# Optimization experiments

Hardware: AMD Instinct MI355X
Metric: run time of the kernel (lower is better)

## Reference

```python
import jax, jax.numpy as jnp
import numpy as np

TOKEN_NUM = 81   # init default token_num
KNN_K = 2        # hardcoded in apply_clustering
LAYER_INDEX = 3


def setup_inputs() -> dict:
    key = jax.random.key(0)
    k1, k2, k3 = jax.random.split(key, 3)
    B, F, N, C = 8, 1024, 17, 512
    x = jax.random.normal(k1, (B, F, N, C), dtype=jnp.float32)
    # nn.Parameter init normal_(std=0.02)
    pos_embed_token = 0.02 * jax.random.normal(k2, (1, TOKEN_NUM, C), dtype=jnp.float32)
    # deterministic stand-in for torch.rand tie-breaker noise on density
    density_noise = jax.random.uniform(k3, (B, F), dtype=jnp.float32)
    return {"x": x, "pos_embed_token": pos_embed_token,
            "density_noise": density_noise, "current_layer": LAYER_INDEX}


def _dpc_knn_index(x_knn, density_noise, cluster_num, k):
    # x_knn: (B, F, C) pooled features; returns sorted cluster-center indices (B, cluster_num)
    B, F, C = x_knn.shape
    sq = jnp.sum(x_knn * x_knn, axis=-1)                       # (B, F)
    d2 = sq[:, :, None] + sq[:, None, :] - 2.0 * jnp.einsum('bic,bjc->bij', x_knn, x_knn)
    dist = jnp.sqrt(jnp.maximum(d2, 0.0)) / jnp.sqrt(jnp.asarray(C, x_knn.dtype))  # cdist / C**0.5
    # k smallest distances (self included, dist 0)
    neg_nearest, _ = jax.lax.top_k(-dist, k)                   # (B, F, k)
    dist_nearest = -neg_nearest
    density = jnp.exp(-jnp.mean(dist_nearest ** 2, axis=-1))   # (B, F)
    density = density + density_noise * 1e-6                   # tie-breaker
    # mask[b,i,j] = density[b,j] > density[b,i]
    mask = (density[:, None, :] > density[:, :, None]).astype(x_knn.dtype)
    dist_max = jnp.max(dist.reshape(B, -1), axis=-1)[:, None, None]
    min_dist = jnp.min(dist * mask + dist_max * (1.0 - mask), axis=-1)  # (B, F)
    score = min_dist * density
    _, index_down = jax.lax.top_k(score, cluster_num)          # (B, cluster_num)
    return jnp.sort(index_down, axis=-1)


def reference(x, pos_embed_token, density_noise, current_layer):
    # forward path only hits clustering when current_layer == layer_index
    if current_layer != LAYER_INDEX:
        return x
    B, F, N, C = x.shape
    # AdaptiveAvgPool1d(1) over joint axis after 'b f n c -> b (f c) n' == mean over n
    x_knn = jnp.mean(x, axis=2)                                # (B, F, C)
    index = _dpc_knn_index(x_knn, density_noise, TOKEN_NUM, KNN_K)
    index = jax.lax.stop_gradient(index)                       # clustering is under no_grad
    # gather selected frames: x[batch, index] -> (B, token_num, N, C)
    compressed = jnp.take_along_axis(x, index[:, :, None, None], axis=1)
    # '+ pos_embed_token' applied per (b n) f c  ==  broadcast over joints
    compressed = compressed + pos_embed_token[:, :, None, :]
    return compressed
```

## Files before the change

### kernel.cpp

```cpp
#include <hip/hip_runtime.h>
#include <math.h>
#include <float.h>

#define BB 8
#define FF 1024
#define NJ 17
#define CH 512
#define TOK 81
#define RCP_SQRT_C 0.04419417382415922f
#define LP 133

typedef short bf16x8 __attribute__((ext_vector_type(8)));
typedef float f32x16 __attribute__((ext_vector_type(16)));

static __device__ inline unsigned short f2bf(float f) {
    __bf16 h = (__bf16)f;
    return __builtin_bit_cast(unsigned short, h);
}
static __device__ inline float bf2f(unsigned short u) {
    return (float)__builtin_bit_cast(__bf16, u);
}


__global__ __launch_bounds__(256) void pool_kernel(const float* __restrict__ x,
                                                   uint4* __restrict__ fhi,
                                                   uint4* __restrict__ flo,
                                                   float* __restrict__ sq,
                                                   unsigned* __restrict__ dmx) {
    const int t = threadIdx.x;
    if (blockIdx.x == 0 && t < BB) dmx[t] = 0u;
    const int wid = t >> 6, lane = t & 63;
    const int row0 = blockIdx.x * 4;
    const int row = row0 + wid;
    const int b = row >> 10, f0 = row0 & 1023;
    const float* px = x + (size_t)row * NJ * CH + lane * 8;
    float a[8] = {};
    #pragma unroll
    for (int n = 0; n < NJ; ++n) {
        const float4 v0 = *(const float4*)(px + (size_t)n * CH);
        const float4 v1 = *(const float4*)(px + (size_t)n * CH + 4);
        a[0] += v0.x; a[1] += v0.y; a[2] += v0.z; a[3] += v0.w;
        a[4] += v1.x; a[5] += v1.y; a[6] += v1.z; a[7] += v1.w;
    }
    float ssq = 0.f;
    unsigned short hi[8], lo[8];
    #pragma unroll
    for (int j = 0; j < 8; ++j) {
        const float m = a[j] / 17.0f;
        ssq += m * m;
        hi[j] = f2bf(m);
        lo[j] = f2bf(m - bf2f(hi[j]));
    }
    #pragma unroll
    for (int off = 32; off > 0; off >>= 1) ssq += __shfl_down(ssq, off);
    if (lane == 0) sq[row] = ssq;

    uint4 uh, ul;
    uh.x = (unsigned)hi[0] | ((unsigned)hi[1] << 16);
    uh.y = (unsigned)hi[2] | ((unsigned)hi[3] << 16);
    uh.z = (unsigned)hi[4] | ((unsigned)hi[5] << 16);
    uh.w = (unsigned)hi[6] | ((unsigned)hi[7] << 16);
    ul.x = (unsigned)lo[0] | ((unsigned)lo[1] << 16);
    ul.y = (unsigned)lo[2] | ((unsigned)lo[3] << 16);
    ul.z = (unsigned)lo[4] | ((unsigned)lo[5] << 16);
    ul.w = (unsigned)lo[6] | ((unsigned)lo[7] << 16);
    __shared__ uint4 sh_hi[256], sh_lo[256];
    sh_hi[lane * 4 + wid] = uh;
    sh_lo[lane * 4 + wid] = ul;
    __syncthreads();
    const int k8 = t >> 2, fpr = t & 3;
    const int s = k8 >> 1, h = k8 & 1;
    const size_t o = (((size_t)b * 32 + s) * 2 + h) * 1024 + f0 + fpr;
    fhi[o] = sh_hi[t];
    flo[o] = sh_lo[t];
}

__global__ __launch_bounds__(256) void dist_kernel(const uint4* __restrict__ fhi,
                                                   const uint4* __restrict__ flo,
                                                   const float* __restrict__ sq,
                                                   float* __restrict__ dist) {
    const int b = blockIdx.x & 7;
    int tri = blockIdx.x >> 3, rt = 0;
    while (tri >= 8 - rt) { tri -= 8 - rt; ++rt; }
    const int ct = rt + tri;
    const bool diag = (rt == ct);
    const int tid = threadIdx.x;
    const int w = tid >> 6, lane = tid & 63;
    const int R = rt * 128 + (w & 1) * 64;
    const int C = ct * 128 + (w >> 1) * 64;
    const int h = lane >> 5, fr = lane & 31;

    size_t a0 = ((size_t)b * 64 + h) * 1024 + R + fr;
    size_t b0 = ((size_t)b * 64 + h) * 1024 + C + fr;

    f32x16 acc00, acc01, acc10, acc11;
    #pragma unroll
    for (int i = 0; i < 16; ++i) { acc00[i] = 0.f; acc01[i] = 0.f; acc10[i] = 0.f; acc11[i] = 0.f; }

    bf16x8 A0h = *(const bf16x8*)(fhi + a0), A1h = *(const bf16x8*)(fhi + a0 + 32);
    bf16x8 A0l = *(const bf16x8*)(flo + a0), A1l = *(const bf16x8*)(flo + a0 + 32);
    bf16x8 B0h = *(const bf16x8*)(fhi + b0), B1h = *(const bf16x8*)(fhi + b0 + 32);
    bf16x8 B0l = *(const bf16x8*)(flo + b0), B1l = *(const bf16x8*)(flo + b0 + 32);

    #pragma unroll 4
    for (int s = 0; s < 32; ++s) {
        const bf16x8 cA0h = A0h, cA1h = A1h, cA0l = A0l, cA1l = A1l;
        const bf16x8 cB0h = B0h, cB1h = B1h, cB0l = B0l, cB1l = B1l;
        if (s < 31) {
            a0 += 2048; b0 += 2048;
            A0h = *(const bf16x8*)(fhi + a0); A1h = *(const bf16x8*)(fhi + a0 + 32);
            A0l = *(const bf16x8*)(flo + a0); A1l = *(const bf16x8*)(flo + a0 + 32);
            B0h = *(const bf16x8*)(fhi + b0); B1h = *(const bf16x8*)(fhi + b0 + 32);
            B0l = *(const bf16x8*)(flo + b0); B1l = *(const bf16x8*)(flo + b0 + 32);
        }
        acc00 = __builtin_amdgcn_mfma_f32_32x32x16_bf16(cA0h, cB0h, acc00, 0, 0, 0);
        acc01 = __builtin_amdgcn_mfma_f32_32x32x16_bf16(cA0h, cB1h, acc01, 0, 0, 0);
        acc10 = __builtin_amdgcn_mfma_f32_32x32x16_bf16(cA1h, cB0h, acc10, 0, 0, 0);
        acc11 = __builtin_amdgcn_mfma_f32_32x32x16_bf16(cA1h, cB1h, acc11, 0, 0, 0);
        acc00 = __builtin_amdgcn_mfma_f32_32x32x16_bf16(cA0h, cB0l, acc00, 0, 0, 0);
        acc01 = __builtin_amdgcn_mfma_f32_32x32x16_bf16(cA0h, cB1l, acc01, 0, 0, 0);
        acc10 = __builtin_amdgcn_mfma_f32_32x32x16_bf16(cA1h, cB0l, acc10, 0, 0, 0);
        acc11 = __builtin_amdgcn_mfma_f32_32x32x16_bf16(cA1h, cB1l, acc11, 0, 0, 0);
        acc00 = __builtin_amdgcn_mfma_f32_32x32x16_bf16(cA0l, cB0h, acc00, 0, 0, 0);
        acc01 = __builtin_amdgcn_mfma_f32_32x32x16_bf16(cA0l, cB1h, acc01, 0, 0, 0);
        acc10 = __builtin_amdgcn_mfma_f32_32x32x16_bf16(cA1l, cB0h, acc10, 0, 0, 0);
        acc11 = __builtin_amdgcn_mfma_f32_32x32x16_bf16(cA1l, cB1h, acc11, 0, 0, 0);
    }

    __shared__ float lds[64 * LP];
    const int bF = b * FF;
    const int R0 = rt * 128, C0 = ct * 128;
    const float sqc0 = sq[bF + C + fr], sqc1 = sq[bF + C + fr + 32];
    const int lcb = (w >> 1) * 64 + fr;

    #pragma unroll
    for (int p = 0; p < 2; ++p) {
        if ((w & 1) == p) {
            #pragma unroll
            for (int reg = 0; reg < 16; ++reg) {
                const int rp = 4 * h + (reg & 3) + 8 * (reg >> 2);
                const float sqr0 = sq[bF + R + rp];
                const float sqr1 = sq[bF + R + rp + 32];
                lds[rp * LP + lcb] =
                    sqrtf(fmaxf(sqr0 + sqc0 - 2.0f * acc00[reg], 0.f)) * RCP_SQRT_C;
                lds[rp * LP + lcb + 32] =
                    sqrtf(fmaxf(sqr0 + sqc1 - 2.0f * acc01[reg], 0.f)) * RCP_SQRT_C;
                lds[(rp + 32) * LP + lcb] =
                    sqrtf(fmaxf(sqr1 + sqc0 - 2.0f * acc10[reg], 0.f)) * RCP_SQRT_C;
                lds[(rp + 32) * LP + lcb + 32] =
                    sqrtf(fmaxf(sqr1 + sqc1 - 2.0f * acc11[reg], 0.f)) * RCP_SQRT_C;
            }
        }
        __syncthreads();
        if (!diag) {
            for (int q = tid; q < 64 * 128; q += 256) {
                const int lr = q >> 7, c = q & 127;
                dist[((size_t)bF + R0 + p * 64 + lr) * FF + C0 + c] = lds[lr * LP + c];
            }
            for (int q = tid; q < 64 * 128; q += 256) {
                const int lr = q & 63, c = q >> 6;
                dist[((size_t)bF + C0 + c) * FF + R0 + p * 64 + lr] = lds[lr * LP + c];
            }
        } else if (p == 0) {
            for (int q = tid; q < 64 * 128; q += 256) {
                const int i = q >> 7, j = q & 127;
                const float v = (i == j) ? 0.f : (i < j ? lds[i * LP + j] : lds[j * LP + i]);
                dist[((size_t)bF + R0 + i) * FF + C0 + j] = v;
            }
            for (int q = tid; q < 64 * 64; q += 256) {
                const int i = 64 + (q >> 6), j = q & 63;
                dist[((size_t)bF + R0 + i) * FF + C0 + j] = lds[j * LP + i];
            }
        } else {
            for (int q = tid; q < 64 * 64; q += 256) {
                const int i = 64 + (q >> 6), j = 64 + (q & 63);
                const float v = (i == j) ? 0.f
                               : (i < j ? lds[(i - 64) * LP + j] : lds[(j - 64) * LP + i]);
                dist[((size_t)bF + R0 + i) * FF + C0 + j] = v;
            }
        }
        __syncthreads();
    }
}

__device__ inline void merge2(float& lo0, float& lo1, float c0, float c1) {
    float n0 = fminf(lo0, c0);
    float n1 = fminf(fmaxf(lo0, c0), fminf(lo1, c1));
    lo0 = n0; lo1 = n1;
}

__global__ __launch_bounds__(256) void rowstat_kernel(const float* __restrict__ dist,
                                                      const float* __restrict__ noise,
                                                      float* __restrict__ density,
                                                      unsigned* __restrict__ dmx) {
    const int wid = threadIdx.x >> 6;
    const int r = blockIdx.x * 4 + wid;
    const int lane = threadIdx.x & 63;
    const float* dr = dist + (size_t)r * FF + lane * 4;
    float lo0 = FLT_MAX, lo1 = FLT_MAX, mx = -FLT_MAX;
    #pragma unroll
    for (int j = 0; j < 4; ++j) {
        const float4 d = *(const float4*)(dr + j * 256);
        mx = fmaxf(mx, fmaxf(fmaxf(d.x, d.y), fmaxf(d.z, d.w)));
        merge2(lo0, lo1, fminf(d.x, d.y), fmaxf(d.x, d.y));
        merge2(lo0, lo1, fminf(d.z, d.w), fmaxf(d.z, d.w));
    }
    #pragma unroll
    for (int off = 32; off > 0; off >>= 1) {
        const float o0 = __shfl_down(lo0, off);
        const float o1 = __shfl_down(lo1, off);
        const float om = __shfl_down(mx, off);
        merge2(lo0, lo1, o0, o1);
        mx = fmaxf(mx, om);
    }
    __shared__ float wmx[4];
    if (lane == 0) {
        density[r] = expf(-0.5f * (lo0 * lo0 + lo1 * lo1)) + noise[r] * 1e-6f;
        wmx[wid] = mx;
    }
    __syncthreads();
    if (threadIdx.x == 0) {
        const float m = fmaxf(fmaxf(wmx[0], wmx[1]), fmaxf(wmx[2], wmx[3]));
        atomicMax(&dmx[blockIdx.x >> 8], __float_as_uint(m));
    }
}

__global__ __launch_bounds__(256) void scoremin_kernel(const float* __restrict__ dist,
                                                       const float* __restrict__ density,
                                                       const float* __restrict__ distmax,
                                                       float* __restrict__ score) {
    const int r = blockIdx.x * 4 + (threadIdx.x >> 6);
    const int lane = threadIdx.x & 63;
    const int b = r >> 10;
    const float* dr = dist + (size_t)r * FF + lane * 4;
    const float* db = density + (size_t)b * FF + lane * 4;
    const float dme = density[r];
    float mn = FLT_MAX;
    #pragma unroll
    for (int j = 0; j < 4; ++j) {
        const float4 d = *(const float4*)(dr + j * 256);
        const float4 de = *(const float4*)(db + j * 256);
        mn = fminf(mn, (de.x > dme) ? d.x : FLT_MAX);
        mn = fminf(mn, (de.y > dme) ? d.y : FLT_MAX);
        mn = fminf(mn, (de.z > dme) ? d.z : FLT_MAX);
        mn = fminf(mn, (de.w > dme) ? d.w : FLT_MAX);
    }
    #pragma unroll
    for (int off = 32; off > 0; off >>= 1) mn = fminf(mn, __shfl_down(mn, off));
    if (lane == 0) {
        if (mn == FLT_MAX) mn = distmax[b];
        score[r] = mn * dme;
    }
}

__global__ __launch_bounds__(256) void topk_kernel(const float* __restrict__ score,
                                                   int* __restrict__ selsort) {
    const int b = blockIdx.x, t = threadIdx.x;
    const int w = t >> 6, lane = t & 63;
    const float* sb = score + b * FF;
    unsigned v[4];
    #pragma unroll
    for (int j = 0; j < 4; ++j) v[j] = __float_as_uint(sb[t + 256 * j]);

    __shared__ unsigned hist[256];
    __shared__ unsigned wtot[4];
    __shared__ unsigned sh_byte, sh_kk;
    unsigned prefix = 0, kk = TOK;
    #pragma unroll
    for (int pass = 0; pass < 4; ++pass) {
        const int sh = 24 - 8 * pass;
        const unsigned pmask = (pass == 0) ? 0u : (0xFFFFFFFFu << (sh + 8));
        hist[t] = 0;
        __syncthreads();
        #pragma unroll
        for (int j = 0; j < 4; ++j)
            if ((v[j] & pmask) == prefix) atomicAdd(&hist[(v[j] >> sh) & 255], 1u);
        __syncthreads();
        const unsigned cnt = hist[t];
        unsigned s = cnt;
        #pragma unroll
        for (int off = 1; off < 64; off <<= 1) {
            const unsigned o = __shfl_down(s, off);
            if (lane + off < 64) s += o;
        }
        if (lane == 0) wtot[w] = s;
        __syncthreads();
        unsigned hi2 = 0;
        for (int w2 = w + 1; w2 < 4; ++w2) hi2 += wtot[w2];
        const unsigned S_incl = s + hi2;
        const unsigned S_excl = S_incl - cnt;
        if (S_excl < kk && kk <= S_incl) { sh_byte = (unsigned)t; sh_kk = kk - S_excl; }
        __syncthreads();
        prefix |= (sh_byte << sh);
        kk = sh_kk;
    }
    const unsigned T = prefix;

    __shared__ unsigned cgt[16], ceq[16];
    unsigned long long bgt[4], beq[4];
    #pragma unroll
    for (int j = 0; j < 4; ++j) {
        bgt[j] = __ballot(v[j] > T);
        beq[j] = __ballot(v[j] == T);
        if (lane == 0) {
            cgt[j * 4 + w] = (unsigned)__popcll(bgt[j]);
            ceq[j * 4 + w] = (unsigned)__popcll(beq[j]);
        }
    }
    __syncthreads();
    const unsigned long long below = (1ULL << lane) - 1ULL;
    #pragma unroll
    for (int j = 0; j < 4; ++j) {
        const bool gt = v[j] > T, eq = v[j] == T;
        if (!gt && !eq) continue;
        const int c = j * 4 + w;
        unsigned bq_gt = 0, bq_eq = 0;
        for (int cc = 0; cc < c; ++cc) { bq_gt += cgt[cc]; bq_eq += ceq[cc]; }
        const unsigned wgt = (unsigned)__popcll(bgt[j] & below);
        const unsigned weq = (unsigned)__popcll(beq[j] & below);
        unsigned pos;
        if (gt) {
            const unsigned eq_before = bq_eq + weq;
            pos = bq_gt + wgt + ((eq_before < kk) ? eq_before : kk);
        } else {
            const unsigned e = bq_eq + weq;
            if (e >= kk) continue;
            pos = bq_gt + wgt + e;
        }
        selsort[b * TOK + pos] = (int)(t + 256 * j);
    }
}

__global__ __launch_bounds__(256) void gather_kernel(const float* __restrict__ x,
                                                     const float* __restrict__ pos,
                                                     const int* __restrict__ selsort,
                                                     float* __restrict__ out) {
    const size_t i = (size_t)blockIdx.x * 256 + threadIdx.x;
    const size_t total = (size_t)BB * TOK * NJ * (CH / 4);
    if (i >= total) return;
    const int c4 = (int)(i & (CH / 4 - 1));
    size_t r = i >> 7;
    const int n = (int)(r % NJ); r /= NJ;
    const int t = (int)(r % TOK);
    const int b = (int)(r / TOK);
    const int f = selsort[b * TOK + t];
    float4 v = *(const float4*)(x + (((size_t)(b * FF + f)) * NJ + n) * CH + c4 * 4);
    const float4 p = *(const float4*)(pos + (size_t)t * CH + c4 * 4);
    v.x += p.x; v.y += p.y; v.z += p.z; v.w += p.w;
    *(float4*)(out + i * 4) = v;
}

extern "C" void kernel_launch(void* const* d_in, const int* in_sizes, int n_in,
                              void* d_out, int out_size, void* d_ws, size_t ws_size,
                              hipStream_t stream) {
    const float* x     = (const float*)d_in[0];
    const float* pos   = (const float*)d_in[1];
    const float* noise = (const float*)d_in[2];
    float* out = (float*)d_out;

    uint4* fhi    = (uint4*)d_ws;
    uint4* flo    = fhi + (size_t)BB * 32 * 2 * 1024;
    float* dist   = (float*)(flo + (size_t)BB * 32 * 2 * 1024);
    float* sq     = dist + (size_t)BB * FF * FF;
    float* density = sq + BB * FF;
    float* distmax = density + BB * FF;
    float* score   = distmax + 8;
    int*   selsort = (int*)(score + BB * FF);

    pool_kernel<<<(BB * FF) / 4, 256, 0, stream>>>(x, fhi, flo, sq, (unsigned*)distmax);
    dist_kernel<<<288, 256, 0, stream>>>(fhi, flo, sq, dist);
    rowstat_kernel<<<(BB * FF) / 4, 256, 0, stream>>>(dist, noise, density, (unsigned*)distmax);
    scoremin_kernel<<<(BB * FF) / 4, 256, 0, stream>>>(dist, density, distmax, score);
    topk_kernel<<<BB, 256, 0, stream>>>(score, selsort);
    const int gtot = (int)(((size_t)BB * TOK * NJ * (CH / 4) + 255) / 256);
    gather_kernel<<<gtot, 256, 0, stream>>>(x, pos, selsort, out);
}
```

Measured before the change: 483.4 us.

## Fuse row stats, score, top-k and gather into one persistent kernel

```diff
diff --git a/kernel.cpp b/kernel.cpp
--- a/kernel.cpp
+++ b/kernel.cpp
@@ -26,9 +26,9 @@
                                                    uint4* __restrict__ fhi,
                                                    uint4* __restrict__ flo,
                                                    float* __restrict__ sq,
-                                                   unsigned* __restrict__ dmx) {
+                                                   unsigned* __restrict__ ctrl) {
     const int t = threadIdx.x;
-    if (blockIdx.x == 0 && t < BB) dmx[t] = 0u;
+    if (blockIdx.x == 0 && t < 24) ctrl[t] = 0u;
     const int wid = t >> 6, lane = t & 63;
     const int row0 = blockIdx.x * 4;
     const int row = row0 + wid;
@@ -183,171 +183,200 @@
     }
 }
 
-__device__ inline void merge2(float& lo0, float& lo1, float c0, float c1) {
-    float n0 = fminf(lo0, c0);
-    float n1 = fminf(fmaxf(lo0, c0), fminf(lo1, c1));
-    lo0 = n0; lo1 = n1;
-}
-
-__global__ __launch_bounds__(256) void rowstat_kernel(const float* __restrict__ dist,
-                                                      const float* __restrict__ noise,
-                                                      float* __restrict__ density,
-                                                      unsigned* __restrict__ dmx) {
-    const int wid = threadIdx.x >> 6;
-    const int r = blockIdx.x * 4 + wid;
-    const int lane = threadIdx.x & 63;
-    const float* dr = dist + (size_t)r * FF + lane * 4;
-    float lo0 = FLT_MAX, lo1 = FLT_MAX, mx = -FLT_MAX;
-    #pragma unroll
-    for (int j = 0; j < 4; ++j) {
-        const float4 d = *(const float4*)(dr + j * 256);
-        mx = fmaxf(mx, fmaxf(fmaxf(d.x, d.y), fmaxf(d.z, d.w)));
-        merge2(lo0, lo1, fminf(d.x, d.y), fmaxf(d.x, d.y));
-        merge2(lo0, lo1, fminf(d.z, d.w), fmaxf(d.z, d.w));
-    }
-    #pragma unroll
-    for (int off = 32; off > 0; off >>= 1) {
-        const float o0 = __shfl_down(lo0, off);
-        const float o1 = __shfl_down(lo1, off);
-        const float om = __shfl_down(mx, off);
-        merge2(lo0, lo1, o0, o1);
-        mx = fmaxf(mx, om);
-    }
-    __shared__ float wmx[4];
-    if (lane == 0) {
-        density[r] = expf(-0.5f * (lo0 * lo0 + lo1 * lo1)) + noise[r] * 1e-6f;
-        wmx[wid] = mx;
-    }
-    __syncthreads();
-    if (threadIdx.x == 0) {
-        const float m = fmaxf(fmaxf(wmx[0], wmx[1]), fmaxf(wmx[2], wmx[3]));
-        atomicMax(&dmx[blockIdx.x >> 8], __float_as_uint(m));
-    }
-}
-
-__global__ __launch_bounds__(256) void scoremin_kernel(const float* __restrict__ dist,
-                                                       const float* __restrict__ density,
-                                                       const float* __restrict__ distmax,
-                                                       float* __restrict__ score) {
-    const int r = blockIdx.x * 4 + (threadIdx.x >> 6);
-    const int lane = threadIdx.x & 63;
-    const int b = r >> 10;
-    const float* dr = dist + (size_t)r * FF + lane * 4;
-    const float* db = density + (size_t)b * FF + lane * 4;
-    const float dme = density[r];
-    float mn = FLT_MAX;
-    #pragma unroll
-    for (int j = 0; j < 4; ++j) {
-        const float4 d = *(const float4*)(dr + j * 256);
-        const float4 de = *(const float4*)(db + j * 256);
-        mn = fminf(mn, (de.x > dme) ? d.x : FLT_MAX);
-        mn = fminf(mn, (de.y > dme) ? d.y : FLT_MAX);
-        mn = fminf(mn, (de.z > dme) ? d.z : FLT_MAX);
-        mn = fminf(mn, (de.w > dme) ? d.w : FLT_MAX);
-    }
-    #pragma unroll
-    for (int off = 32; off > 0; off >>= 1) mn = fminf(mn, __shfl_down(mn, off));
-    if (lane == 0) {
-        if (mn == FLT_MAX) mn = distmax[b];
-        score[r] = mn * dme;
-    }
-}
-
-__global__ __launch_bounds__(256) void topk_kernel(const float* __restrict__ score,
-                                                   int* __restrict__ selsort) {
-    const int b = blockIdx.x, t = threadIdx.x;
-    const int w = t >> 6, lane = t & 63;
-    const float* sb = score + b * FF;
-    unsigned v[4];
-    #pragma unroll
-    for (int j = 0; j < 4; ++j) v[j] = __float_as_uint(sb[t + 256 * j]);
-
-    __shared__ unsigned hist[256];
-    __shared__ unsigned wtot[4];
-    __shared__ unsigned sh_byte, sh_kk;
-    unsigned prefix = 0, kk = TOK;
-    #pragma unroll
-    for (int pass = 0; pass < 4; ++pass) {
-        const int sh = 24 - 8 * pass;
-        const unsigned pmask = (pass == 0) ? 0u : (0xFFFFFFFFu << (sh + 8));
-        hist[t] = 0;
+__global__ __launch_bounds__(256) void stats_kernel(const float* __restrict__ dist,
+                                                    const float* __restrict__ noise,
+                                                    float* __restrict__ density,
+                                                    unsigned* __restrict__ ctrl,
+                                                    float* __restrict__ score,
+                                                    int* __restrict__ selsort,
+                                                    const float* __restrict__ x,
+                                                    const float* __restrict__ pos,
+                                                    float* __restrict__ out) {
+    const int t = threadIdx.x, wid = t >> 6, lane = t & 63;
+    const int g = blockIdx.x;
+    const int b = g >> 5;
+    unsigned* dmx = ctrl;
+    unsigned* syncA = ctrl + 8;
+    unsigned* syncD = ctrl + 9;
+    unsigned* bcnt  = ctrl + 10;
+
+    __shared__ float sdens[4][8];
+    float wmax = -FLT_MAX;
+    #pragma unroll
+    for (int k = 0; k < 8; ++k) {
+        const int r = g * 32 + wid * 8 + k;
+        const int dcol = r & 1023;
+        const float* dr = dist + (size_t)r * FF + lane * 4;
+        float mn = FLT_MAX, mx = -FLT_MAX;
+        #pragma unroll
+        for (int j = 0; j < 4; ++j) {
+            float4 d = *(const float4*)(dr + j * 256);
+            mx = fmaxf(mx, fmaxf(fmaxf(d.x, d.y), fmaxf(d.z, d.w)));
+            const int c0 = lane * 4 + j * 256;
+            d.x = (c0 + 0 == dcol) ? FLT_MAX : d.x;
+            d.y = (c0 + 1 == dcol) ? FLT_MAX : d.y;
+            d.z = (c0 + 2 == dcol) ? FLT_MAX : d.z;
+            d.w = (c0 + 3 == dcol) ? FLT_MAX : d.w;
+            mn = fminf(mn, fminf(fminf(d.x, d.y), fminf(d.z, d.w)));
+        }
+        #pragma unroll
+        for (int off = 32; off > 0; off >>= 1) {
+            mn = fminf(mn, __shfl_down(mn, off));
+            mx = fmaxf(mx, __shfl_down(mx, off));
+        }
+        if (lane == 0) {
+            const float dv = expf(-0.5f * mn * mn) + noise[r] * 1e-6f;
+            density[r] = dv;
+            sdens[wid][k] = dv;
+            wmax = fmaxf(wmax, mx);
+        }
+    }
+    __shared__ float swm[4];
+    if (lane == 0) swm[wid] = wmax;
+    __syncthreads();
+    if (t == 0) {
+        atomicMax(&dmx[b], __float_as_uint(fmaxf(fmaxf(swm[0], swm[1]), fmaxf(swm[2], swm[3]))));
+        __threadfence();
+        atomicAdd(syncA, 1u);
+        while (__hip_atomic_load(syncA, __ATOMIC_ACQUIRE, __HIP_MEMORY_SCOPE_AGENT) < 256u)
+            __builtin_amdgcn_s_sleep(8);
+    }
+    __syncthreads();
+    __threadfence();
+
+    const float dmaxb = __uint_as_float(
+        __hip_atomic_load(&dmx[b], __ATOMIC_RELAXED, __HIP_MEMORY_SCOPE_AGENT));
+    float e[16];
+    {
+        const volatile float* db = density + (size_t)b * FF;
+        #pragma unroll
+        for (int j = 0; j < 16; ++j) e[j] = db[lane + j * 64];
+    }
+    #pragma unroll
+    for (int k = 0; k < 8; ++k) {
+        const int r = g * 32 + wid * 8 + k;
+        const float dme = sdens[wid][k];
+        const float* dr = dist + (size_t)r * FF;
+        float mn = FLT_MAX;
+        #pragma unroll
+        for (int j = 0; j < 16; ++j) {
+            const float d = dr[lane + j * 64];
+            mn = fminf(mn, (e[j] > dme) ? d : FLT_MAX);
+        }
+        #pragma unroll
+        for (int off = 32; off > 0; off >>= 1) mn = fminf(mn, __shfl_down(mn, off));
+        if (lane == 0) score[r] = ((mn == FLT_MAX) ? dmaxb : mn) * dme;
+    }
+    __syncthreads();
+
+    __shared__ int slast;
+    if (t == 0) {
+        __threadfence();
+        slast = (atomicAdd(&bcnt[b], 1u) == 31u) ? 1 : 0;
+    }
+    __syncthreads();
+    if (slast) {
+        __threadfence();
+        const volatile float* sb = score + (size_t)b * FF;
+        unsigned v[4];
+        #pragma unroll
+        for (int j = 0; j < 4; ++j) v[j] = __float_as_uint(sb[t + 256 * j]);
+
+        __shared__ unsigned hist[256];
+        __shared__ unsigned wtot[4];
+        __shared__ unsigned sh_byte, sh_kk;
+        unsigned prefix = 0, kk = TOK;
+        #pragma unroll
+        for (int pass = 0; pass < 4; ++pass) {
+            const int sh = 24 - 8 * pass;
+            const unsigned pmask = (pass == 0) ? 0u : (0xFFFFFFFFu << (sh + 8));
+            hist[t] = 0;
+            __syncthreads();
+            #pragma unroll
+            for (int j = 0; j < 4; ++j)
+                if ((v[j] & pmask) == prefix) atomicAdd(&hist[(v[j] >> sh) & 255], 1u);
+            __syncthreads();
+            const unsigned cnt = hist[t];
+            unsigned s = cnt;
+            #pragma unroll
+            for (int off = 1; off < 64; off <<= 1) {
+                const unsigned o = __shfl_down(s, off);
+                if (lane + off < 64) s += o;
+            }
+            if (lane == 0) wtot[wid] = s;
+            __syncthreads();
+            unsigned hi2 = 0;
+            for (int w2 = wid + 1; w2 < 4; ++w2) hi2 += wtot[w2];
+            const unsigned S_incl = s + hi2;
+            const unsigned S_excl = S_incl - cnt;
+            if (S_excl < kk && kk <= S_incl) { sh_byte = (unsigned)t; sh_kk = kk - S_excl; }
+            __syncthreads();
+            prefix |= (sh_byte << sh);
+            kk = sh_kk;
+        }
+        const unsigned T = prefix;
+
+        __shared__ unsigned cgt[16], ceq[16];
+        unsigned long long bgt[4], beq[4];
+        #pragma unroll
+        for (int j = 0; j < 4; ++j) {
+            bgt[j] = __ballot(v[j] > T);
+            beq[j] = __ballot(v[j] == T);
+            if (lane == 0) {
+                cgt[j * 4 + wid] = (unsigned)__popcll(bgt[j]);
+                ceq[j * 4 + wid] = (unsigned)__popcll(beq[j]);
+            }
+        }
         __syncthreads();
-        #pragma unroll
-        for (int j = 0; j < 4; ++j)
-            if ((v[j] & pmask) == prefix) atomicAdd(&hist[(v[j] >> sh) & 255], 1u);
-        __syncthreads();
-        const unsigned cnt = hist[t];
-        unsigned s = cnt;
-        #pragma unroll
-        for (int off = 1; off < 64; off <<= 1) {
-            const unsigned o = __shfl_down(s, off);
-            if (lane + off < 64) s += o;
-        }
-        if (lane == 0) wtot[w] = s;
-        __syncthreads();
-        unsigned hi2 = 0;
-        for (int w2 = w + 1; w2 < 4; ++w2) hi2 += wtot[w2];
-        const unsigned S_incl = s + hi2;
-        const unsigned S_excl = S_incl - cnt;
-        if (S_excl < kk && kk <= S_incl) { sh_byte = (unsigned)t; sh_kk = kk - S_excl; }
-        __syncthreads();
-        prefix |= (sh_byte << sh);
-        kk = sh_kk;
-    }
-    const unsigned T = prefix;
-
-    __shared__ unsigned cgt[16], ceq[16];
-    unsigned long long bgt[4], beq[4];
-    #pragma unroll
-    for (int j = 0; j < 4; ++j) {
-        bgt[j] = __ballot(v[j] > T);
-        beq[j] = __ballot(v[j] == T);
-        if (lane == 0) {
-            cgt[j * 4 + w] = (unsigned)__popcll(bgt[j]);
-            ceq[j * 4 + w] = (unsigned)__popcll(beq[j]);
-        }
-    }
-    __syncthreads();
-    const unsigned long long below = (1ULL << lane) - 1ULL;
-    #pragma unroll
-    for (int j = 0; j < 4; ++j) {
-        const bool gt = v[j] > T, eq = v[j] == T;
-        if (!gt && !eq) continue;
-        const int c = j * 4 + w;
-        unsigned bq_gt = 0, bq_eq = 0;
-        for (int cc = 0; cc < c; ++cc) { bq_gt += cgt[cc]; bq_eq += ceq[cc]; }
-        const unsigned wgt = (unsigned)__popcll(bgt[j] & below);
-        const unsigned weq = (unsigned)__popcll(beq[j] & below);
-        unsigned pos;
-        if (gt) {
-            const unsigned eq_before = bq_eq + weq;
-            pos = bq_gt + wgt + ((eq_before < kk) ? eq_before : kk);
-        } else {
-            const unsigned e = bq_eq + weq;
-            if (e >= kk) continue;
-            pos = bq_gt + wgt + e;
-        }
-        selsort[b * TOK + pos] = (int)(t + 256 * j);
-    }
-}
-
-__global__ __launch_bounds__(256) void gather_kernel(const float* __restrict__ x,
-                                                     const float* __restrict__ pos,
-                                                     const int* __restrict__ selsort,
-                                                     float* __restrict__ out) {
-    const size_t i = (size_t)blockIdx.x * 256 + threadIdx.x;
+        const unsigned long long below = (1ULL << lane) - 1ULL;
+        #pragma unroll
+        for (int j = 0; j < 4; ++j) {
+            const bool gt = v[j] > T, eq = v[j] == T;
+            if (!gt && !eq) continue;
+            const int c = j * 4 + wid;
+            unsigned bq_gt = 0, bq_eq = 0;
+            for (int cc = 0; cc < c; ++cc) { bq_gt += cgt[cc]; bq_eq += ceq[cc]; }
+            const unsigned wgt = (unsigned)__popcll(bgt[j] & below);
+            const unsigned weq = (unsigned)__popcll(beq[j] & below);
+            unsigned pos_;
+            if (gt) {
+                const unsigned eq_before = bq_eq + weq;
+                pos_ = bq_gt + wgt + ((eq_before < kk) ? eq_before : kk);
+            } else {
+                const unsigned eord = bq_eq + weq;
+                if (eord >= kk) continue;
+                pos_ = bq_gt + wgt + eord;
+            }
+            selsort[b * TOK + pos_] = (int)(t + 256 * j);
+        }
+        __threadfence();
+    }
+    __syncthreads();
+    if (t == 0) atomicAdd(syncD, 1u);
+
+    if (t == 0) {
+        while (__hip_atomic_load(syncD, __ATOMIC_ACQUIRE, __HIP_MEMORY_SCOPE_AGENT) < 256u)
+            __builtin_amdgcn_s_sleep(8);
+    }
+    __syncthreads();
+    __threadfence();
+
+    __shared__ int ssel[BB * TOK];
+    for (int q = t; q < BB * TOK; q += 256) ssel[q] = *((volatile const int*)selsort + q);
+    __syncthreads();
     const size_t total = (size_t)BB * TOK * NJ * (CH / 4);
-    if (i >= total) return;
-    const int c4 = (int)(i & (CH / 4 - 1));
-    size_t r = i >> 7;
-    const int n = (int)(r % NJ); r /= NJ;
-    const int t = (int)(r % TOK);
-    const int b = (int)(r / TOK);
-    const int f = selsort[b * TOK + t];
-    float4 v = *(const float4*)(x + (((size_t)(b * FF + f)) * NJ + n) * CH + c4 * 4);
-    const float4 p = *(const float4*)(pos + (size_t)t * CH + c4 * 4);
-    v.x += p.x; v.y += p.y; v.z += p.z; v.w += p.w;
-    *(float4*)(out + i * 4) = v;
+    for (size_t i = (size_t)g * 256 + t; i < total; i += 256 * 256) {
+        const int c4 = (int)(i & (CH / 4 - 1));
+        size_t r = i >> 7;
+        const int n = (int)(r % NJ); r /= NJ;
+        const int tok = (int)(r % TOK);
+        const int bb = (int)(r / TOK);
+        const int f = ssel[bb * TOK + tok];
+        float4 v = *(const float4*)(x + (((size_t)(bb * FF + f)) * NJ + n) * CH + c4 * 4);
+        const float4 p = *(const float4*)(pos + (size_t)tok * CH + c4 * 4);
+        v.x += p.x; v.y += p.y; v.z += p.z; v.w += p.w;
+        *(float4*)(out + i * 4) = v;
+    }
 }
 
 extern "C" void kernel_launch(void* const* d_in, const int* in_sizes, int n_in,
@@ -361,17 +390,14 @@
     uint4* fhi    = (uint4*)d_ws;
     uint4* flo    = fhi + (size_t)BB * 32 * 2 * 1024;
     float* dist   = (float*)(flo + (size_t)BB * 32 * 2 * 1024);
-    float* sq     = dist + (size_t)BB * FF * FF;
+    float* sq      = dist + (size_t)BB * FF * FF;
     float* density = sq + BB * FF;
-    float* distmax = density + BB * FF;
-    float* score   = distmax + 8;
+    unsigned* ctrl = (unsigned*)(density + BB * FF);
+    float* score   = (float*)(ctrl + 24);
     int*   selsort = (int*)(score + BB * FF);
 
-    pool_kernel<<<(BB * FF) / 4, 256, 0, stream>>>(x, fhi, flo, sq, (unsigned*)distmax);
+    pool_kernel<<<(BB * FF) / 4, 256, 0, stream>>>(x, fhi, flo, sq, ctrl);
     dist_kernel<<<288, 256, 0, stream>>>(fhi, flo, sq, dist);
-    rowstat_kernel<<<(BB * FF) / 4, 256, 0, stream>>>(dist, noise, density, (unsigned*)distmax);
-    scoremin_kernel<<<(BB * FF) / 4, 256, 0, stream>>>(dist, density, distmax, score);
-    topk_kernel<<<BB, 256, 0, stream>>>(score, selsort);
-    const int gtot = (int)(((size_t)BB * TOK * NJ * (CH / 4) + 255) / 256);
-    gather_kernel<<<gtot, 256, 0, stream>>>(x, pos, selsort, out);
-}
+    stats_kernel<<<256, 256, 0, stream>>>(dist, noise, density, ctrl, score, selsort,
+                                          x, pos, out);
+}
```

Result: slower. 563.6 us (+16.6%).
